# Optimization experiments

Hardware: AMD Instinct MI355X
Metric: run time of the kernel (lower is better)

The kernel has to match this reference:

```python
import jax, jax.numpy as jnp
import numpy as np


def _sage_conv(x, src, dst, W_l, b_l, W_r, num_nodes):
    # PyG SAGEConv (aggr='mean'): out = lin_l(mean_j x[src_j]) + lin_r(x)
    msg = x[src]                                                  # [E, d]
    agg = jax.ops.segment_sum(msg, dst, num_segments=num_nodes)   # [N, d]
    deg = jax.ops.segment_sum(jnp.ones_like(dst, dtype=x.dtype), dst,
                              num_segments=num_nodes)             # [N]
    mean = agg / jnp.maximum(deg, 1.0)[:, None]
    return mean @ W_l + b_l + x @ W_r


def setup_inputs() -> dict:
    key = jax.random.key(0)
    ks = jax.random.split(key, 8)
    N, E, D = 50000, 640000, 128
    s = 1.0 / np.sqrt(D)
    return {
        "x": jax.random.normal(ks[0], (N, D), dtype=jnp.float32),
        "edge_index": jax.random.randint(ks[1], (2, E), 0, N, dtype=jnp.int64),
        "W1_l": jax.random.normal(ks[2], (D, D), dtype=jnp.float32) * s,
        "b1_l": jnp.zeros((D,), dtype=jnp.float32),
        "W1_r": jax.random.normal(ks[3], (D, D), dtype=jnp.float32) * s,
        "W2_l": jax.random.normal(ks[4], (D, D), dtype=jnp.float32) * s,
        "b2_l": jnp.zeros((D,), dtype=jnp.float32),
        "W2_r": jax.random.normal(ks[5], (D, D), dtype=jnp.float32) * s,
    }


def reference(x, edge_index, W1_l, b1_l, W1_r, W2_l, b2_l, W2_r):
    N = x.shape[0]
    src, dst = edge_index[0], edge_index[1]
    h = jax.nn.relu(_sage_conv(x, src, dst, W1_l, b1_l, W1_r, N))
    z = _sage_conv(h, src, dst, W2_l, b2_l, W2_r, N)
    return z
```

## Files before the change

kernel.cpp:

```cpp
#include <hip/hip_runtime.h>
#include <hip/hip_bf16.h>


#define CAP 64
#define NBLKA 128

#if __has_builtin(__builtin_amdgcn_global_load_lds)
#define HAS_GLDS 1
#endif

typedef __attribute__((ext_vector_type(8))) short short8v;
typedef __attribute__((ext_vector_type(4))) float float4v;

__device__ __forceinline__ ushort f2bf(float f) {
    unsigned u = __float_as_uint(f);
    u += 0x7fff + ((u >> 16) & 1);
    return (ushort)(u >> 16);
}
__device__ __forceinline__ float bflo(unsigned v) { return __uint_as_float(v << 16); }
__device__ __forceinline__ float bfhi(unsigned v) { return __uint_as_float(v & 0xffff0000u); }

#if __has_builtin(__builtin_amdgcn_cvt_pk_fp8_f32) && __has_builtin(__builtin_amdgcn_cvt_f32_fp8)
#define HW_FP8 1
#endif

__device__ __forceinline__ float fp8_dec_sw(unsigned b) {
    unsigned s = b >> 7, e = (b >> 3) & 15, m = b & 7;
    float v = e ? __uint_as_float(((e + 120u) << 23) | (m << 20))
                : (float)m * 0.001953125f;
    return s ? -v : v;
}
__device__ __forceinline__ unsigned fp8_enc_sw(float f) {
    float aa = fabsf(f);
    unsigned e32 = __float_as_uint(aa) >> 23;
    float c = (aa < 0.015625f) ? 16384.f : __uint_as_float((e32 + 20) << 23);
    float r = (aa + c) - c;
    if (r > 448.f) r = 448.f;
    unsigned s = (__float_as_uint(f) >> 31) << 7;
    if (r == 0.f) return s;
    unsigned u = __float_as_uint(r);
    int e = (int)(u >> 23) - 127;
    if (e < -6) return s | (unsigned)(r * 512.f);
    return s | ((unsigned)(e + 7) << 3) | ((u >> 20) & 7);
}

__device__ __forceinline__ unsigned enc4_fp8(float4 v) {
#ifdef HW_FP8
    int p = 0;
    p = __builtin_amdgcn_cvt_pk_fp8_f32(v.x, v.y, p, false);
    p = __builtin_amdgcn_cvt_pk_fp8_f32(v.z, v.w, p, true);
    return (unsigned)p;
#else
    return fp8_enc_sw(v.x) | (fp8_enc_sw(v.y) << 8) |
           (fp8_enc_sw(v.z) << 16) | (fp8_enc_sw(v.w) << 24);
#endif
}
__device__ __forceinline__ unsigned char enc1_fp8(float v) {
#ifdef HW_FP8
    return (unsigned char)(__builtin_amdgcn_cvt_pk_fp8_f32(v, v, 0, false) & 0xff);
#else
    return (unsigned char)fp8_enc_sw(v);
#endif
}
template <int SEL>
__device__ __forceinline__ float dec_fp8(unsigned w) {
#ifdef HW_FP8
    return __builtin_amdgcn_cvt_f32_fp8(w, SEL);
#else
    return fp8_dec_sw((w >> (SEL * 8)) & 0xff);
#endif
}
__device__ __forceinline__ void acc4_fp8(float* a, unsigned w) {
    a[0] += dec_fp8<0>(w);
    a[1] += dec_fp8<1>(w);
    a[2] += dec_fp8<2>(w);
    a[3] += dec_fp8<3>(w);
}

__global__ __launch_bounds__(256) void prep_bin_kernel(
    const int* __restrict__ src, const int* __restrict__ dst, int E, int N, int nbuk,
    unsigned* __restrict__ seg, int* __restrict__ cntA,
    const float* __restrict__ X, ushort* __restrict__ Xb,
    unsigned* __restrict__ X8, int n4,
    const float* __restrict__ W1l, const float* __restrict__ W1r, ushort* __restrict__ Wt1,
    const float* __restrict__ W2l, const float* __restrict__ W2r, ushort* __restrict__ Wt2,
    int nConv) {
    int b = blockIdx.x;
    if (b < NBLKA) {
        __shared__ int cnt[512];
        for (int i = threadIdx.x; i < nbuk; i += 256) cnt[i] = 0;
        __syncthreads();
        const int EPB = ((E + NBLKA - 1) / NBLKA + 3) & ~3;
        const int e0 = b * EPB;
        const int e1 = min(E & ~3, e0 + EPB);
        const int4* d4p = reinterpret_cast<const int4*>(dst);
        const int4* s4p = reinterpret_cast<const int4*>(src);
        unsigned* myseg = seg + (size_t)b * nbuk * CAP;
        for (int e4 = (e0 >> 2) + threadIdx.x; e4 < (e1 >> 2); e4 += 256) {
            int4 d4 = d4p[e4];
            int4 s4 = s4p[e4];
#pragma unroll
            for (int j = 0; j < 4; ++j) {
                int d = (&d4.x)[j];
                int bu = d >> 8;
                int pos = atomicAdd(&cnt[bu], 1);
                if (pos < CAP)
                    myseg[bu * CAP + pos] =
                        ((unsigned)(d & 255) << 16) | (unsigned)((&s4.x)[j] & 0xffff);
            }
        }
        if (b == 0) {
            int t = threadIdx.x;
            if (t < (E & 3)) {
                int e = (E & ~3) + t;
                int d = dst[e];
                int bu = d >> 8;
                int pos = atomicAdd(&cnt[bu], 1);
                if (pos < CAP)
                    myseg[bu * CAP + pos] =
                        ((unsigned)(d & 255) << 16) | (unsigned)(src[e] & 0xffff);
            }
        }
        __syncthreads();
        for (int i = threadIdx.x; i < nbuk; i += 256)
            cntA[b * nbuk + i] = min(cnt[i], CAP);
    } else if (b < NBLKA + nConv) {
        int i = (b - NBLKA) * 256 + threadIdx.x;
        if (i < n4) {
            float4 v = reinterpret_cast<const float4*>(X)[i];
            ushort4 o;
            o.x = f2bf(v.x); o.y = f2bf(v.y); o.z = f2bf(v.z); o.w = f2bf(v.w);
            reinterpret_cast<ushort4*>(Xb)[i] = o;
            X8[i] = enc4_fp8(v);
        }
    } else {
        int wb = b - NBLKA - nConv;
        const float* Wl = (wb < 128) ? W1l : W2l;
        const float* Wr = (wb < 128) ? W1r : W2r;
        ushort* Wt = (wb < 128) ? Wt1 : Wt2;
        int col = wb & 127;
        int k = threadIdx.x;
        float v = (k < 128) ? Wl[k * 128 + col] : Wr[(k - 128) * 128 + col];
        int gr = k >> 3, sub = k & 7;
        Wt[(size_t)(col * 32 + (gr ^ (col & 7))) * 8 + sub] = f2bf(v);
    }
}

__global__ __launch_bounds__(256) void csr_build_kernel(
    const unsigned* __restrict__ seg, const int* __restrict__ cntA,
    ushort* __restrict__ csrc, int* __restrict__ cursor, int N, int nbuk) {
    __shared__ ushort lcs[256 * CAP];
    __shared__ int lcnt[256];
    __shared__ int scnt[NBLKA];
    const int b = blockIdx.x;
    const int tid = threadIdx.x;
    lcnt[tid] = 0;
    if (tid < NBLKA) scnt[tid] = cntA[tid * nbuk + b];
    __syncthreads();
    for (int idx = tid; idx < NBLKA * CAP; idx += 256) {
        int blk = idx >> 6, slot = idx & (CAP - 1);
        if (slot < scnt[blk]) {
            unsigned en = seg[((size_t)blk * nbuk + b) * CAP + slot];
            int local = (en >> 16) & 255;
            int pos = atomicAdd(&lcnt[local], 1);
            if (pos < CAP) lcs[local * CAP + pos] = (ushort)(en & 0xffff);
        }
    }
    __syncthreads();
    const int maxNode = min(256, N - b * 256);
    const uint4* s4 = reinterpret_cast<const uint4*>(lcs);
    uint4* d4 = reinterpret_cast<uint4*>(csrc + (size_t)b * 256 * CAP);
    for (int i = tid; i < maxNode * (CAP / 8); i += 256) d4[i] = s4[i];
    if (tid < maxNode) cursor[b * 256 + tid] = min(lcnt[tid], CAP);
}

__global__ __launch_bounds__(256) void gather_mean_fp8(
    const unsigned* __restrict__ X8, const int* __restrict__ cnt,
    const ushort* __restrict__ csrc, ushort* __restrict__ meanb, int N) {
    const int wid = __builtin_amdgcn_readfirstlane((blockIdx.x * 256 + threadIdx.x) >> 6);
    if (wid >= N) return;
    const int lane = threadIdx.x & 63;
    const int q = lane >> 4;
    const int lq = lane & 15;
    const int dc = min(cnt[wid], CAP);
    const ushort* ep = csrc + (size_t)wid * CAP;

    float acc[8];
#pragma unroll
    for (int j = 0; j < 8; ++j) acc[j] = 0.f;

    const uint2* Xp = reinterpret_cast<const uint2*>(X8);
    int e = 0;
#pragma unroll 4
    for (; e + 3 < dc; e += 4) {
        uint2 iw = *reinterpret_cast<const uint2*>(ep + e);
        unsigned wv = (q & 2) ? iw.y : iw.x;
        int s = (q & 1) ? (int)(wv >> 16) : (int)(wv & 0xffff);
        uint2 v = Xp[(size_t)s * 16 + lq];
        acc4_fp8(acc, v.x);
        acc4_fp8(acc + 4, v.y);
    }
    if (e + q < dc) {
        int s = ep[e + q];
        uint2 v = Xp[(size_t)s * 16 + lq];
        acc4_fp8(acc, v.x);
        acc4_fp8(acc + 4, v.y);
    }

#pragma unroll
    for (int j = 0; j < 8; ++j) {
        acc[j] += __shfl_xor(acc[j], 32);
        acc[j] += __shfl_xor(acc[j], 16);
    }

    if (q == 0) {
        float sc = 1.0f / (float)max(dc, 1);
        uint4 o;
        o.x = (unsigned)f2bf(acc[0] * sc) | ((unsigned)f2bf(acc[1] * sc) << 16);
        o.y = (unsigned)f2bf(acc[2] * sc) | ((unsigned)f2bf(acc[3] * sc) << 16);
        o.z = (unsigned)f2bf(acc[4] * sc) | ((unsigned)f2bf(acc[5] * sc) << 16);
        o.w = (unsigned)f2bf(acc[6] * sc) | ((unsigned)f2bf(acc[7] * sc) << 16);
        reinterpret_cast<uint4*>(meanb)[(size_t)wid * 16 + lq] = o;
    }
}

__global__ __launch_bounds__(256) void sage_layer1_fused(
    const ushort* __restrict__ A0,
    const ushort* __restrict__ A1,
    const ushort* __restrict__ Wt1,
    const ushort* __restrict__ Wt2,
    const float* __restrict__ b1, const float* __restrict__ b2,
    unsigned char* __restrict__ p2_8,
    ushort* __restrict__ s2,
    int N) {
    __shared__ __align__(16) ushort Ws[128 * 256];
    __shared__ __align__(16) ushort Hs[64 * 128];
    const int tid = threadIdx.x;
    const int lane = tid & 63;
    const int wave = tid >> 6;
    const int r = lane & 15;
    const int g = lane >> 4;
    const int rt0 = blockIdx.x * 64 + wave * 16;

    int ar = rt0 + r;
    if (ar >= N) ar = N - 1;

#ifdef HAS_GLDS
    {
        auto gp = (const __attribute__((address_space(1))) char*)(const char*)Wt1;
        auto lp = (__attribute__((address_space(3))) char*)(char*)Ws;
#pragma unroll
        for (int it = 0; it < 16; ++it) {
            int G = it * 256 + tid;
            int Lw = (it * 256 + (tid & 192)) * 16;
            __builtin_amdgcn_global_load_lds(gp + (size_t)G * 16, lp + Lw, 16, 0, 0);
        }
    }
#else
    {
        const uint4* Wg = reinterpret_cast<const uint4*>(Wt1);
        uint4* Ls = reinterpret_cast<uint4*>(Ws);
#pragma unroll
        for (int it = 0; it < 16; ++it) { int G = it * 256 + tid; Ls[G] = Wg[G]; }
    }
#endif

    short8v af[8];
#pragma unroll
    for (int ks = 0; ks < 8; ++ks) {
        const ushort* Ap = ((ks < 4) ? A0 : A1) + (size_t)ar * 128;
        af[ks] = *(const short8v*)(Ap + (ks & 3) * 32 + g * 8);
    }

    float4v acc[8];
#pragma unroll
    for (int ct = 0; ct < 8; ++ct) {
        float bv = b1[ct * 16 + r];
        acc[ct] = (float4v){bv, bv, bv, bv};
    }

    __syncthreads();

#pragma unroll
    for (int ks = 0; ks < 8; ++ks) {
#pragma unroll
        for (int ct = 0; ct < 8; ++ct) {
            const int col = ct * 16 + r;
            const int gr = (ks * 4 + g) ^ (r & 7);
            short8v bf = *(const short8v*)(Ws + col * 256 + gr * 8);
            acc[ct] = __builtin_amdgcn_mfma_f32_16x16x32_bf16(af[ks], bf, acc[ct], 0, 0, 0);
        }
    }

    {
        ushort* hw = Hs + wave * 16 * 128;
#pragma unroll
        for (int ct = 0; ct < 8; ++ct) {
            const int col = ct * 16 + r;
            const int g0 = col >> 3;
#pragma unroll
            for (int reg = 0; reg < 4; ++reg) {
                const int row = g * 4 + reg;
                float v = fmaxf(acc[ct][reg], 0.f);
                hw[row * 128 + ((g0 ^ (row & 7)) * 8 + (col & 7))] = f2bf(v);
            }
        }
    }

    __syncthreads();

#ifdef HAS_GLDS
    {
        auto gp = (const __attribute__((address_space(1))) char*)(const char*)Wt2;
        auto lp = (__attribute__((address_space(3))) char*)(char*)Ws;
#pragma unroll
        for (int it = 0; it < 16; ++it) {
            int G = it * 256 + tid;
            int Lw = (it * 256 + (tid & 192)) * 16;
            __builtin_amdgcn_global_load_lds(gp + (size_t)G * 16, lp + Lw, 16, 0, 0);
        }
    }
#else
    {
        const uint4* Wg = reinterpret_cast<const uint4*>(Wt2);
        uint4* Ls = reinterpret_cast<uint4*>(Ws);
#pragma unroll
        for (int it = 0; it < 16; ++it) { int G = it * 256 + tid; Ls[G] = Wg[G]; }
    }
#endif

    short8v ah[4];
    {
        const ushort* hw = Hs + wave * 16 * 128;
#pragma unroll
        for (int ks = 0; ks < 4; ++ks) {
            const int gr = (ks * 4 + g) ^ (r & 7);
            ah[ks] = *(const short8v*)(hw + r * 128 + gr * 8);
        }
    }

    float4v accp[8], accs[8];
#pragma unroll
    for (int ct = 0; ct < 8; ++ct) {
        float bv = b2[ct * 16 + r];
        accp[ct] = (float4v){0.f, 0.f, 0.f, 0.f};
        accs[ct] = (float4v){bv, bv, bv, bv};
    }

    __syncthreads();

#pragma unroll
    for (int ks = 0; ks < 4; ++ks) {
#pragma unroll
        for (int ct = 0; ct < 8; ++ct) {
            const int col = ct * 16 + r;
            const int grp = (ks * 4 + g) ^ (r & 7);
            const int grs = 16 + (((ks + 4 - 4) * 4 + g) ^ (r & 7));
            short8v bp = *(const short8v*)(Ws + col * 256 + grp * 8);
            short8v bs = *(const short8v*)(Ws + col * 256 + grs * 8);
            accp[ct] = __builtin_amdgcn_mfma_f32_16x16x32_bf16(ah[ks], bp, accp[ct], 0, 0, 0);
            accs[ct] = __builtin_amdgcn_mfma_f32_16x16x32_bf16(ah[ks], bs, accs[ct], 0, 0, 0);
        }
    }

#pragma unroll
    for (int ct = 0; ct < 8; ++ct) {
        const int col = ct * 16 + r;
#pragma unroll
        for (int reg = 0; reg < 4; ++reg) {
            int orow = rt0 + g * 4 + reg;
            if (orow < N) {
                p2_8[(size_t)orow * 128 + col] = enc1_fp8(accp[ct][reg]);
                s2[(size_t)orow * 128 + col] = f2bf(accs[ct][reg]);
            }
        }
    }
}

__global__ __launch_bounds__(256) void gather_final(
    const unsigned* __restrict__ P8, const int* __restrict__ cnt,
    const ushort* __restrict__ csrc, const ushort* __restrict__ s2,
    float* __restrict__ out, int N) {
    const int wid = __builtin_amdgcn_readfirstlane((blockIdx.x * 256 + threadIdx.x) >> 6);
    if (wid >= N) return;
    const int lane = threadIdx.x & 63;
    const int q = lane >> 4;
    const int lq = lane & 15;
    const int dc = min(cnt[wid], CAP);
    const ushort* ep = csrc + (size_t)wid * CAP;

    float acc[8];
#pragma unroll
    for (int j = 0; j < 8; ++j) acc[j] = 0.f;

    const uint2* Xp = reinterpret_cast<const uint2*>(P8);
    int e = 0;
#pragma unroll 4
    for (; e + 3 < dc; e += 4) {
        uint2 iw = *reinterpret_cast<const uint2*>(ep + e);
        unsigned wv = (q & 2) ? iw.y : iw.x;
        int s = (q & 1) ? (int)(wv >> 16) : (int)(wv & 0xffff);
        uint2 v = Xp[(size_t)s * 16 + lq];
        acc4_fp8(acc, v.x);
        acc4_fp8(acc + 4, v.y);
    }
    if (e + q < dc) {
        int s = ep[e + q];
        uint2 v = Xp[(size_t)s * 16 + lq];
        acc4_fp8(acc, v.x);
        acc4_fp8(acc + 4, v.y);
    }

#pragma unroll
    for (int j = 0; j < 8; ++j) {
        acc[j] += __shfl_xor(acc[j], 32);
        acc[j] += __shfl_xor(acc[j], 16);
    }

    if (q == 0) {
        float sc = 1.0f / (float)max(dc, 1);
        uint4 sv = reinterpret_cast<const uint4*>(s2)[(size_t)wid * 16 + lq];
        float4 o0, o1;
        o0.x = acc[0] * sc + bflo(sv.x); o0.y = acc[1] * sc + bfhi(sv.x);
        o0.z = acc[2] * sc + bflo(sv.y); o0.w = acc[3] * sc + bfhi(sv.y);
        o1.x = acc[4] * sc + bflo(sv.z); o1.y = acc[5] * sc + bfhi(sv.z);
        o1.z = acc[6] * sc + bflo(sv.w); o1.w = acc[7] * sc + bfhi(sv.w);
        float4* op = reinterpret_cast<float4*>(out + (size_t)wid * 128 + lq * 8);
        op[0] = o0;
        op[1] = o1;
    }
}


extern "C" void kernel_launch(void* const* d_in, const int* in_sizes, int n_in,
                              void* d_out, int out_size, void* d_ws, size_t ws_size,
                              hipStream_t stream) {
    const float* x   = (const float*)d_in[0];
    const int*   ei  = (const int*)d_in[1];
    const float* W1l = (const float*)d_in[2];
    const float* b1  = (const float*)d_in[3];
    const float* W1r = (const float*)d_in[4];
    const float* W2l = (const float*)d_in[5];
    const float* b2  = (const float*)d_in[6];
    const float* W2r = (const float*)d_in[7];
    float* out = (float*)d_out;

    const int D = 128;
    const int N = in_sizes[0] / D;
    const int E = in_sizes[1] / 2;
    const int nbuk = (N + 255) >> 8;

    const int* srcp = ei;
    const int* dstp = ei + E;

    char* ws = (char*)d_ws;
    ushort*   xb     = (ushort*)ws;
    ushort*   meanb  = xb + (size_t)N * D;
    ushort*   s2     = meanb + (size_t)N * D;
    ushort*   Wt1    = s2 + (size_t)N * D;
    ushort*   Wt2    = Wt1 + 128 * 256;
    unsigned* x8     = (unsigned*)(Wt2 + 128 * 256);
    unsigned* p2_8   = x8 + (size_t)N * D / 4;
    ushort*   csrc   = (ushort*)(p2_8 + (size_t)N * D / 4);
    int*      cursor = (int*)(csrc + (size_t)N * CAP);
    unsigned* seg    = (unsigned*)(cursor + ((N + 3) & ~3));
    int*      cntA   = (int*)(seg + (size_t)NBLKA * nbuk * CAP);

    const int n4 = N * D / 4;
    const int nConv = (n4 + 255) / 256;

    prep_bin_kernel<<<NBLKA + nConv + 256, 256, 0, stream>>>(
        srcp, dstp, E, N, nbuk, seg, cntA, x, xb, x8, n4,
        W1l, W1r, Wt1, W2l, W2r, Wt2, nConv);

    csr_build_kernel<<<nbuk, 256, 0, stream>>>(seg, cntA, csrc, cursor, N, nbuk);

    const int gather_blocks = (N * 64 + 255) / 256;

    gather_mean_fp8<<<gather_blocks, 256, 0, stream>>>(x8, cursor, csrc, meanb, N);

    sage_layer1_fused<<<(N + 63) / 64, 256, 0, stream>>>(
        meanb, xb, Wt1, Wt2, b1, b2, (unsigned char*)p2_8, s2, N);

    gather_final<<<gather_blocks, 256, 0, stream>>>(p2_8, cursor, csrc, s2, out, N);
}
```

Baseline: 97.79 us.

## Split gather kernels into feature halves with 8 edges per wave iteration

Both gather kernels are merged into one templated kernel that runs two grid halves, each block covering 64 of the 128 fp8 feature bytes per node. Each wave now processes 8 edges in parallel, one per lane octet, which doubles memory-level parallelism per iteration. The cost is that every node's edge indices are read twice. Outputs are now written with nontemporal stores to avoid polluting the cache. An extra shuffle stage is added to the reduction.

```diff
diff --git a/kernel.cpp b/kernel.cpp
--- a/kernel.cpp
+++ b/kernel.cpp
@@ -11,6 +11,19 @@
 
 typedef __attribute__((ext_vector_type(8))) short short8v;
 typedef __attribute__((ext_vector_type(4))) float float4v;
+typedef __attribute__((ext_vector_type(4))) unsigned uint4v;
+
+#if __has_builtin(__builtin_nontemporal_store)
+__device__ __forceinline__ void nt_store_u4(uint4v v, uint4v* p) {
+    __builtin_nontemporal_store(v, p);
+}
+__device__ __forceinline__ void nt_store_f4(float4v v, float4v* p) {
+    __builtin_nontemporal_store(v, p);
+}
+#else
+__device__ __forceinline__ void nt_store_u4(uint4v v, uint4v* p) { *p = v; }
+__device__ __forceinline__ void nt_store_f4(float4v v, float4v* p) { *p = v; }
+#endif
 
 __device__ __forceinline__ ushort f2bf(float f) {
     unsigned u = __float_as_uint(f);
@@ -174,14 +187,20 @@
     if (tid < maxNode) cursor[b * 256 + tid] = min(lcnt[tid], CAP);
 }
 
-__global__ __launch_bounds__(256) void gather_mean_fp8(
+template <int FINAL>
+__global__ __launch_bounds__(256) void gather_half(
     const unsigned* __restrict__ X8, const int* __restrict__ cnt,
-    const ushort* __restrict__ csrc, ushort* __restrict__ meanb, int N) {
-    const int wid = __builtin_amdgcn_readfirstlane((blockIdx.x * 256 + threadIdx.x) >> 6);
+    const ushort* __restrict__ csrc, const ushort* __restrict__ s2,
+    void* __restrict__ outv, int N, int nblk_half) {
+    int b = blockIdx.x;
+    const int half = (b >= nblk_half) ? 1 : 0;
+    b -= half * nblk_half;
+    const int tid = threadIdx.x;
+    const int wid = __builtin_amdgcn_readfirstlane((b * 256 + tid) >> 6);
     if (wid >= N) return;
-    const int lane = threadIdx.x & 63;
-    const int q = lane >> 4;
-    const int lq = lane & 15;
+    const int lane = tid & 63;
+    const int oct = lane >> 3;
+    const int l8 = lane & 7;
     const int dc = min(cnt[wid], CAP);
     const ushort* ep = csrc + (size_t)wid * CAP;
 
@@ -191,18 +210,18 @@
 
     const uint2* Xp = reinterpret_cast<const uint2*>(X8);
     int e = 0;
-#pragma unroll 4
-    for (; e + 3 < dc; e += 4) {
-        uint2 iw = *reinterpret_cast<const uint2*>(ep + e);
-        unsigned wv = (q & 2) ? iw.y : iw.x;
-        int s = (q & 1) ? (int)(wv >> 16) : (int)(wv & 0xffff);
-        uint2 v = Xp[(size_t)s * 16 + lq];
+    for (; e + 7 < dc; e += 8) {
+        uint4 iw = *reinterpret_cast<const uint4*>(ep + e);
+        unsigned wv = (oct & 4) ? ((oct & 2) ? iw.w : iw.z)
+                                : ((oct & 2) ? iw.y : iw.x);
+        int s = (oct & 1) ? (int)(wv >> 16) : (int)(wv & 0xffff);
+        uint2 v = Xp[(size_t)s * 16 + half * 8 + l8];
         acc4_fp8(acc, v.x);
         acc4_fp8(acc + 4, v.y);
     }
-    if (e + q < dc) {
-        int s = ep[e + q];
-        uint2 v = Xp[(size_t)s * 16 + lq];
+    if (e + oct < dc) {
+        int s = ep[e + oct];
+        uint2 v = Xp[(size_t)s * 16 + half * 8 + l8];
         acc4_fp8(acc, v.x);
         acc4_fp8(acc + 4, v.y);
     }
@@ -211,16 +230,31 @@
     for (int j = 0; j < 8; ++j) {
         acc[j] += __shfl_xor(acc[j], 32);
         acc[j] += __shfl_xor(acc[j], 16);
-    }
-
-    if (q == 0) {
+        acc[j] += __shfl_xor(acc[j], 8);
+    }
+
+    if (oct == 0) {
         float sc = 1.0f / (float)max(dc, 1);
-        uint4 o;
-        o.x = (unsigned)f2bf(acc[0] * sc) | ((unsigned)f2bf(acc[1] * sc) << 16);
-        o.y = (unsigned)f2bf(acc[2] * sc) | ((unsigned)f2bf(acc[3] * sc) << 16);
-        o.z = (unsigned)f2bf(acc[4] * sc) | ((unsigned)f2bf(acc[5] * sc) << 16);
-        o.w = (unsigned)f2bf(acc[6] * sc) | ((unsigned)f2bf(acc[7] * sc) << 16);
-        reinterpret_cast<uint4*>(meanb)[(size_t)wid * 16 + lq] = o;
+        if (!FINAL) {
+            uint4v o;
+            o.x = (unsigned)f2bf(acc[0] * sc) | ((unsigned)f2bf(acc[1] * sc) << 16);
+            o.y = (unsigned)f2bf(acc[2] * sc) | ((unsigned)f2bf(acc[3] * sc) << 16);
+            o.z = (unsigned)f2bf(acc[4] * sc) | ((unsigned)f2bf(acc[5] * sc) << 16);
+            o.w = (unsigned)f2bf(acc[6] * sc) | ((unsigned)f2bf(acc[7] * sc) << 16);
+            nt_store_u4(o, reinterpret_cast<uint4v*>((ushort*)outv) +
+                               (size_t)wid * 16 + half * 8 + l8);
+        } else {
+            uint4 sv = reinterpret_cast<const uint4*>(s2)[(size_t)wid * 16 + half * 8 + l8];
+            float4v o0, o1;
+            o0.x = acc[0] * sc + bflo(sv.x); o0.y = acc[1] * sc + bfhi(sv.x);
+            o0.z = acc[2] * sc + bflo(sv.y); o0.w = acc[3] * sc + bfhi(sv.y);
+            o1.x = acc[4] * sc + bflo(sv.z); o1.y = acc[5] * sc + bfhi(sv.z);
+            o1.z = acc[6] * sc + bflo(sv.w); o1.w = acc[7] * sc + bfhi(sv.w);
+            float4v* op = reinterpret_cast<float4v*>((float*)outv) +
+                          (size_t)wid * 32 + half * 16 + l8 * 2;
+            nt_store_f4(o0, op);
+            nt_store_f4(o1, op + 1);
+        }
     }
 }
 
@@ -355,7 +389,7 @@
         for (int ct = 0; ct < 8; ++ct) {
             const int col = ct * 16 + r;
             const int grp = (ks * 4 + g) ^ (r & 7);
-            const int grs = 16 + (((ks + 4 - 4) * 4 + g) ^ (r & 7));
+            const int grs = 16 + ((ks * 4 + g) ^ (r & 7));
             short8v bp = *(const short8v*)(Ws + col * 256 + grp * 8);
             short8v bs = *(const short8v*)(Ws + col * 256 + grs * 8);
             accp[ct] = __builtin_amdgcn_mfma_f32_16x16x32_bf16(ah[ks], bp, accp[ct], 0, 0, 0);
@@ -374,60 +408,6 @@
                 s2[(size_t)orow * 128 + col] = f2bf(accs[ct][reg]);
             }
         }
-    }
-}
-
-__global__ __launch_bounds__(256) void gather_final(
-    const unsigned* __restrict__ P8, const int* __restrict__ cnt,
-    const ushort* __restrict__ csrc, const ushort* __restrict__ s2,
-    float* __restrict__ out, int N) {
-    const int wid = __builtin_amdgcn_readfirstlane((blockIdx.x * 256 + threadIdx.x) >> 6);
-    if (wid >= N) return;
-    const int lane = threadIdx.x & 63;
-    const int q = lane >> 4;
-    const int lq = lane & 15;
-    const int dc = min(cnt[wid], CAP);
-    const ushort* ep = csrc + (size_t)wid * CAP;
-
-    float acc[8];
-#pragma unroll
-    for (int j = 0; j < 8; ++j) acc[j] = 0.f;
-
-    const uint2* Xp = reinterpret_cast<const uint2*>(P8);
-    int e = 0;
-#pragma unroll 4
-    for (; e + 3 < dc; e += 4) {
-        uint2 iw = *reinterpret_cast<const uint2*>(ep + e);
-        unsigned wv = (q & 2) ? iw.y : iw.x;
-        int s = (q & 1) ? (int)(wv >> 16) : (int)(wv & 0xffff);
-        uint2 v = Xp[(size_t)s * 16 + lq];
-        acc4_fp8(acc, v.x);
-        acc4_fp8(acc + 4, v.y);
-    }
-    if (e + q < dc) {
-        int s = ep[e + q];
-        uint2 v = Xp[(size_t)s * 16 + lq];
-        acc4_fp8(acc, v.x);
-        acc4_fp8(acc + 4, v.y);
-    }
-
-#pragma unroll
-    for (int j = 0; j < 8; ++j) {
-        acc[j] += __shfl_xor(acc[j], 32);
-        acc[j] += __shfl_xor(acc[j], 16);
-    }
-
-    if (q == 0) {
-        float sc = 1.0f / (float)max(dc, 1);
-        uint4 sv = reinterpret_cast<const uint4*>(s2)[(size_t)wid * 16 + lq];
-        float4 o0, o1;
-        o0.x = acc[0] * sc + bflo(sv.x); o0.y = acc[1] * sc + bfhi(sv.x);
-        o0.z = acc[2] * sc + bflo(sv.y); o0.w = acc[3] * sc + bfhi(sv.y);
-        o1.x = acc[4] * sc + bflo(sv.z); o1.y = acc[5] * sc + bfhi(sv.z);
-        o1.z = acc[6] * sc + bflo(sv.w); o1.w = acc[7] * sc + bfhi(sv.w);
-        float4* op = reinterpret_cast<float4*>(out + (size_t)wid * 128 + lq * 8);
-        op[0] = o0;
-        op[1] = o1;
     }
 }
 
@@ -475,12 +455,14 @@
 
     csr_build_kernel<<<nbuk, 256, 0, stream>>>(seg, cntA, csrc, cursor, N, nbuk);
 
-    const int gather_blocks = (N * 64 + 255) / 256;
-
-    gather_mean_fp8<<<gather_blocks, 256, 0, stream>>>(x8, cursor, csrc, meanb, N);
+    const int nblk_half = (N + 3) / 4;
+
+    gather_half<0><<<2 * nblk_half, 256, 0, stream>>>(
+        x8, cursor, csrc, nullptr, meanb, N, nblk_half);
 
     sage_layer1_fused<<<(N + 63) / 64, 256, 0, stream>>>(
         meanb, xb, Wt1, Wt2, b1, b2, (unsigned char*)p2_8, s2, N);
 
-    gather_final<<<gather_blocks, 256, 0, stream>>>(p2_8, cursor, csrc, s2, out, N);
-}
+    gather_half<1><<<2 * nblk_half, 256, 0, stream>>>(
+        p2_8, cursor, csrc, s2, out, N, nblk_half);
+}
```

After: 131.6 us. 1.35x slower.
